# Kernel tuning notes

Measured on AMD Instinct MI355X. Metric: run time of the kernel, lower is better.

Reference implementation:

```python
import jax, jax.numpy as jnp
import numpy as np

B, D, H, E, TOPK = 8192, 1024, 4096, 8, 2


def setup_inputs() -> dict:
    key = jax.random.key(0)
    ks = jax.random.split(key, 5)
    s_in = 1.0 / np.sqrt(D)
    s_h = 1.0 / np.sqrt(H)
    return {
        "x": jax.random.normal(ks[0], (B, D), jnp.float32),
        "Wg": jax.random.normal(ks[1], (D, E), jnp.float32) * s_in,
        "bg": jnp.zeros((E,), jnp.float32),
        "W1": jax.random.normal(ks[2], (E, D, H), jnp.float32) * s_in,
        "b1": jnp.zeros((E, H), jnp.float32),
        "W2": jax.random.normal(ks[3], (E, H, D), jnp.float32) * s_h,
        "b2": jnp.zeros((E, D), jnp.float32),
    }


def reference(x, Wg, bg, W1, b1, W2, b2):
    # Gating: softmax over experts, top-k, renormalize selected weights
    logits = x @ Wg + bg                              # [B, E]
    weights = jax.nn.softmax(logits, axis=-1)
    topw, topi = jax.lax.top_k(weights, TOPK)         # [B, k]
    topw = topw / jnp.sum(topw, axis=-1, keepdims=True)
    # Dense combine weights: [B, E], zero for unselected experts
    comb = jnp.sum(topw[..., None] * jax.nn.one_hot(topi, E, dtype=x.dtype), axis=1)
    # Expert MLPs computed batched per expert (grouped GEMM form)
    h = jax.nn.gelu(jnp.einsum('bd,edh->ebh', x, W1) + b1[:, None, :], approximate=False)  # [E,B,H]
    y = jnp.einsum('ebh,ehd->ebd', h, W2) + b2[:, None, :]                                 # [E,B,D]
    # Weighted combine: only top-k experts have nonzero weight
    out = jnp.einsum('ebd,be->bd', y, comb)           # [B, D]
    return out
```

## Files before the change

kernel.cpp:

```cpp
#include <hip/hip_runtime.h>
#include <stdint.h>

#define B_TOK 8192
#define DDIM 1024
#define HDIM 4096
#define NEXP 8

typedef __bf16 bf16x8 __attribute__((ext_vector_type(8)));
typedef float f32x4 __attribute__((ext_vector_type(4)));

__device__ __forceinline__ unsigned short f2bf(float f) {
  unsigned int u = __float_as_uint(f);
  u += 0x7fffu + ((u >> 16) & 1u);
  return (unsigned short)(u >> 16);
}
__device__ __forceinline__ float bfhi(unsigned int u) {
  return __uint_as_float(u & 0xffff0000u);
}
__device__ __forceinline__ float bflo(unsigned int u) {
  return __uint_as_float(u << 16);
}

__device__ __forceinline__ void gld16(const void* g, void* l) {
  __builtin_amdgcn_global_load_lds(
      (const __attribute__((address_space(1))) void*)g,
      (__attribute__((address_space(3))) void*)l, 16, 0, 0);
}

__device__ __forceinline__ float gelu_f(float v) {
  float u = v * (0.7978845608f + 0.0356774081f * v * v);
  float ex = __expf(2.f * u);
  float th = 1.f - 2.f * __builtin_amdgcn_rcpf(ex + 1.f);
  return 0.5f * v * (1.f + th);
}

__global__ __launch_bounds__(256) void gating_kernel(
    const float* __restrict__ x, const float* __restrict__ Wg,
    const float* __restrict__ bg, int* __restrict__ t2e,
    float* __restrict__ t2w, int* __restrict__ cnt) {
  __shared__ float sWg[NEXP * DDIM];
  int tid = threadIdx.x;
  for (int i = tid; i < NEXP * DDIM; i += 256) {
    int d = i >> 3, e = i & 7;
    sWg[e * DDIM + d] = Wg[i];
  }
  __syncthreads();
  int lane = tid & 63, wave = tid >> 6;
  for (int t = 0; t < 16; ++t) {
    int b = blockIdx.x * 64 + wave * 16 + t;
    float acc[NEXP];
#pragma unroll
    for (int e = 0; e < NEXP; ++e) acc[e] = 0.f;
    const float* xr = x + (size_t)b * DDIM;
#pragma unroll
    for (int j = 0; j < 4; ++j) {
      int d0 = j * 256 + lane * 4;
      float4 xv = *(const float4*)(xr + d0);
#pragma unroll
      for (int e = 0; e < NEXP; ++e) {
        float4 wv = *(const float4*)(sWg + e * DDIM + d0);
        acc[e] += xv.x * wv.x + xv.y * wv.y + xv.z * wv.z + xv.w * wv.w;
      }
    }
#pragma unroll
    for (int off = 32; off > 0; off >>= 1) {
#pragma unroll
      for (int e = 0; e < NEXP; ++e) acc[e] += __shfl_xor(acc[e], off);
    }
    if (lane == 0) {
      float l0[NEXP];
#pragma unroll
      for (int e = 0; e < NEXP; ++e) l0[e] = acc[e] + bg[e];
      int i1 = 0;
      float v1 = l0[0];
#pragma unroll
      for (int e = 1; e < NEXP; ++e)
        if (l0[e] > v1) { v1 = l0[e]; i1 = e; }
      int i2 = (i1 == 0) ? 1 : 0;
      float v2 = l0[i2];
#pragma unroll
      for (int e = 0; e < NEXP; ++e)
        if (e != i1 && l0[e] > v2) { v2 = l0[e]; i2 = e; }
      float w1 = 1.f / (1.f + expf(v2 - v1));
      float w2 = 1.f - w1;
      t2e[b * 2] = i1;
      t2e[b * 2 + 1] = i2;
      t2w[b * 2] = w1;
      t2w[b * 2 + 1] = w2;
      atomicAdd(&cnt[i1], 1);
      atomicAdd(&cnt[i2], 1);
    }
  }
}

__global__ void prefix_kernel(const int* __restrict__ cnt, int* __restrict__ offs,
                              int* __restrict__ tileE, int* __restrict__ tileM,
                              int* __restrict__ ntile) {
  int s = 0, t = 0;
  offs[0] = 0;
  for (int e = 0; e < NEXP; ++e) {
    int c = cnt[e];
    for (int m = 0; m < c; m += 128) { tileE[t] = e; tileM[t] = m; ++t; }
    s += c;
    offs[e + 1] = s;
  }
  *ntile = t;
}

__global__ __launch_bounds__(256) void scatter_kernel(
    const int* __restrict__ t2e, const int* __restrict__ offs,
    int* __restrict__ cursor, int* __restrict__ tok, int* __restrict__ rowpos) {
  int b = blockIdx.x * 256 + threadIdx.x;
  if (b >= B_TOK) return;
#pragma unroll
  for (int k = 0; k < 2; ++k) {
    int e = t2e[b * 2 + k];
    int pos = offs[e] + atomicAdd(&cursor[e], 1);
    tok[pos] = b;
    rowpos[b * 2 + k] = pos;
  }
}

__global__ __launch_bounds__(256) void cvt_x_kernel(const float* __restrict__ x,
                                                    unsigned short* __restrict__ xb) {
  size_t i = ((size_t)blockIdx.x * 256 + threadIdx.x) * 4;
  float4 v = *(const float4*)(x + i);
  ushort4 o;
  o.x = f2bf(v.x);
  o.y = f2bf(v.y);
  o.z = f2bf(v.z);
  o.w = f2bf(v.w);
  *(ushort4*)(xb + i) = o;
}

__global__ __launch_bounds__(256) void transpose_cvt_kernel(
    const float* __restrict__ src, unsigned short* __restrict__ dst, int R, int C) {
  __shared__ unsigned short T[64][72];
  size_t eo = (size_t)blockIdx.z * (size_t)R * C;
  int c0 = blockIdx.x * 64, r0 = blockIdx.y * 64;
  int tid = threadIdx.x;
#pragma unroll
  for (int p = 0; p < 4; ++p) {
    int idx = p * 256 + tid;
    int r = idx >> 4, c4 = (idx & 15) * 4;
    float4 v = *(const float4*)(src + eo + (size_t)(r0 + r) * C + c0 + c4);
    T[r][c4] = f2bf(v.x);
    T[r][c4 + 1] = f2bf(v.y);
    T[r][c4 + 2] = f2bf(v.z);
    T[r][c4 + 3] = f2bf(v.w);
  }
  __syncthreads();
#pragma unroll
  for (int p = 0; p < 2; ++p) {
    int idx = p * 256 + tid;
    int c = idx >> 3, s8 = (idx & 7) * 8;
    ushort4 a, b;
    a.x = T[s8][c];     a.y = T[s8 + 1][c]; a.z = T[s8 + 2][c]; a.w = T[s8 + 3][c];
    b.x = T[s8 + 4][c]; b.y = T[s8 + 5][c]; b.z = T[s8 + 6][c]; b.w = T[s8 + 7][c];
    unsigned short* dp = dst + eo + (size_t)(c0 + c) * R + r0 + s8;
    *(ushort4*)dp = a;
    *(ushort4*)(dp + 4) = b;
  }
}

__global__ __launch_bounds__(256) void gemm1_kernel(
    const unsigned short* __restrict__ xb, const unsigned short* __restrict__ w1t,
    const float* __restrict__ b1, const int* __restrict__ offs,
    const int* __restrict__ tileE, const int* __restrict__ tileM,
    const int* __restrict__ ntile, const int* __restrict__ tok,
    unsigned short* __restrict__ hbuf) {
  int ty = blockIdx.y;
  if (ty >= *ntile) return;
  int e = tileE[ty], m0 = tileM[ty];
  int r0 = offs[e], rows = offs[e + 1] - r0;
  int n0 = blockIdx.x * 128;

  __shared__ __attribute__((aligned(16))) unsigned short Ws[128 * 32];
  __shared__ __attribute__((aligned(16))) unsigned short Xs[128 * 32];

  int tid = threadIdx.x, lane = tid & 63, wave = tid >> 6;
  int u0 = wave * 2, u1 = u0 + 1;
  int sr = lane >> 2, sk = (lane & 3) * 8;
  int nr0 = u0 * 16 + sr, nr1 = u1 * 16 + sr;
  const unsigned short* pW0 = w1t + ((size_t)e * HDIM + n0 + nr0) * DDIM + sk;
  const unsigned short* pW1 = w1t + ((size_t)e * HDIM + n0 + nr1) * DDIM + sk;
  int ma0 = min(m0 + nr0, rows - 1), ma1 = min(m0 + nr1, rows - 1);
  const unsigned short* pX0 = xb + (size_t)tok[r0 + ma0] * DDIM + sk;
  const unsigned short* pX1 = xb + (size_t)tok[r0 + ma1] * DDIM + sk;

  f32x4 acc[4][4];
#pragma unroll
  for (int i = 0; i < 4; ++i)
#pragma unroll
    for (int j = 0; j < 4; ++j) acc[i][j] = (f32x4){0.f, 0.f, 0.f, 0.f};

  int wn = wave & 1, wm = wave >> 1;
  int nbase = wn * 64, mbase = wm * 64;
  int fr = lane & 15, quad = lane >> 4;

  for (int kk = 0; kk < DDIM; kk += 32) {
    gld16(pW0 + kk, Ws + u0 * 512);
    gld16(pW1 + kk, Ws + u1 * 512);
    gld16(pX0 + kk, Xs + u0 * 512);
    gld16(pX1 + kk, Xs + u1 * 512);
    __syncthreads();
    bf16x8 a[4], b[4];
#pragma unroll
    for (int i = 0; i < 4; ++i) {
      a[i] = *(const bf16x8*)(Ws + (size_t)(nbase + i * 16 + fr) * 32 + quad * 8);
      b[i] = *(const bf16x8*)(Xs + (size_t)(mbase + i * 16 + fr) * 32 + quad * 8);
    }
#pragma unroll
    for (int i = 0; i < 4; ++i)
#pragma unroll
      for (int j = 0; j < 4; ++j)
        acc[i][j] = __builtin_amdgcn_mfma_f32_16x16x32_bf16(a[i], b[j], acc[i][j], 0, 0, 0);
    __syncthreads();
  }

  const float* b1e = b1 + (size_t)e * HDIM + n0 + nbase;
  float4 bias[4];
#pragma unroll
  for (int i = 0; i < 4; ++i) bias[i] = *(const float4*)(b1e + i * 16 + quad * 4);
#pragma unroll
  for (int j = 0; j < 4; ++j) {
    int grow = m0 + mbase + j * 16 + fr;
    if (grow < rows) {
      unsigned short* hp = hbuf + (size_t)(r0 + grow) * HDIM + n0 + nbase;
#pragma unroll
      for (int i = 0; i < 4; ++i) {
        ushort4 o;
        o.x = f2bf(gelu_f(acc[i][j][0] + bias[i].x));
        o.y = f2bf(gelu_f(acc[i][j][1] + bias[i].y));
        o.z = f2bf(gelu_f(acc[i][j][2] + bias[i].z));
        o.w = f2bf(gelu_f(acc[i][j][3] + bias[i].w));
        *(ushort4*)(hp + i * 16 + quad * 4) = o;
      }
    }
  }
}

__global__ __launch_bounds__(256) void gemm2_kernel(
    const unsigned short* __restrict__ hbuf, const unsigned short* __restrict__ w2t,
    const float* __restrict__ b2, const int* __restrict__ offs,
    const int* __restrict__ tileE, const int* __restrict__ tileM,
    const int* __restrict__ ntile, unsigned short* __restrict__ ybuf) {
  int ty = blockIdx.y;
  if (ty >= *ntile) return;
  int e = tileE[ty], m0 = tileM[ty];
  int r0 = offs[e], rows = offs[e + 1] - r0;
  int n0 = blockIdx.x * 128;

  __shared__ __attribute__((aligned(16))) unsigned short Ws[128 * 32];
  __shared__ __attribute__((aligned(16))) unsigned short Hs[128 * 32];

  int tid = threadIdx.x, lane = tid & 63, wave = tid >> 6;
  int u0 = wave * 2, u1 = u0 + 1;
  int sr = lane >> 2, sk = (lane & 3) * 8;
  int nr0 = u0 * 16 + sr, nr1 = u1 * 16 + sr;
  const unsigned short* pW0 = w2t + ((size_t)e * DDIM + n0 + nr0) * HDIM + sk;
  const unsigned short* pW1 = w2t + ((size_t)e * DDIM + n0 + nr1) * HDIM + sk;
  const unsigned short* pH0 = hbuf + (size_t)(r0 + min(m0 + nr0, rows - 1)) * HDIM + sk;
  const unsigned short* pH1 = hbuf + (size_t)(r0 + min(m0 + nr1, rows - 1)) * HDIM + sk;

  f32x4 acc[4][4];
#pragma unroll
  for (int i = 0; i < 4; ++i)
#pragma unroll
    for (int j = 0; j < 4; ++j) acc[i][j] = (f32x4){0.f, 0.f, 0.f, 0.f};

  int wn = wave & 1, wm = wave >> 1;
  int nbase = wn * 64, mbase = wm * 64;
  int fr = lane & 15, quad = lane >> 4;

  for (int kk = 0; kk < HDIM; kk += 32) {
    gld16(pW0 + kk, Ws + u0 * 512);
    gld16(pW1 + kk, Ws + u1 * 512);
    gld16(pH0 + kk, Hs + u0 * 512);
    gld16(pH1 + kk, Hs + u1 * 512);
    __syncthreads();
    bf16x8 a[4], b[4];
#pragma unroll
    for (int i = 0; i < 4; ++i) {
      a[i] = *(const bf16x8*)(Ws + (size_t)(nbase + i * 16 + fr) * 32 + quad * 8);
      b[i] = *(const bf16x8*)(Hs + (size_t)(mbase + i * 16 + fr) * 32 + quad * 8);
    }
#pragma unroll
    for (int i = 0; i < 4; ++i)
#pragma unroll
      for (int j = 0; j < 4; ++j)
        acc[i][j] = __builtin_amdgcn_mfma_f32_16x16x32_bf16(a[i], b[j], acc[i][j], 0, 0, 0);
    __syncthreads();
  }

  const float* b2e = b2 + (size_t)e * DDIM + n0 + nbase;
  float4 bias[4];
#pragma unroll
  for (int i = 0; i < 4; ++i) bias[i] = *(const float4*)(b2e + i * 16 + quad * 4);
#pragma unroll
  for (int j = 0; j < 4; ++j) {
    int grow = m0 + mbase + j * 16 + fr;
    if (grow < rows) {
      unsigned short* yp = ybuf + (size_t)(r0 + grow) * DDIM + n0 + nbase;
#pragma unroll
      for (int i = 0; i < 4; ++i) {
        ushort4 o;
        o.x = f2bf(acc[i][j][0] + bias[i].x);
        o.y = f2bf(acc[i][j][1] + bias[i].y);
        o.z = f2bf(acc[i][j][2] + bias[i].z);
        o.w = f2bf(acc[i][j][3] + bias[i].w);
        *(ushort4*)(yp + i * 16 + quad * 4) = o;
      }
    }
  }
}

__global__ __launch_bounds__(256) void combine_kernel(
    const unsigned short* __restrict__ ybuf, const int* __restrict__ rowpos,
    const float* __restrict__ t2w, float* __restrict__ out) {
  int idx = blockIdx.x * 256 + threadIdx.x;
  int b = idx >> 7;
  int c8 = (idx & 127) * 8;
  int p0 = rowpos[b * 2], p1 = rowpos[b * 2 + 1];
  float w0 = t2w[b * 2], w1 = t2w[b * 2 + 1];
  uint4 ya = *(const uint4*)(ybuf + (size_t)p0 * DDIM + c8);
  uint4 yb = *(const uint4*)(ybuf + (size_t)p1 * DDIM + c8);
  float4 o0, o1;
  o0.x = w0 * bflo(ya.x) + w1 * bflo(yb.x);
  o0.y = w0 * bfhi(ya.x) + w1 * bfhi(yb.x);
  o0.z = w0 * bflo(ya.y) + w1 * bflo(yb.y);
  o0.w = w0 * bfhi(ya.y) + w1 * bfhi(yb.y);
  o1.x = w0 * bflo(ya.z) + w1 * bflo(yb.z);
  o1.y = w0 * bfhi(ya.z) + w1 * bfhi(yb.z);
  o1.z = w0 * bflo(ya.w) + w1 * bflo(yb.w);
  o1.w = w0 * bfhi(ya.w) + w1 * bfhi(yb.w);
  float* op = out + (size_t)b * DDIM + c8;
  *(float4*)op = o0;
  *(float4*)(op + 4) = o1;
}

extern "C" void kernel_launch(void* const* d_in, const int* in_sizes, int n_in,
                              void* d_out, int out_size, void* d_ws, size_t ws_size,
                              hipStream_t stream) {
  const float* x = (const float*)d_in[0];
  const float* Wg = (const float*)d_in[1];
  const float* bg = (const float*)d_in[2];
  const float* W1 = (const float*)d_in[3];
  const float* b1 = (const float*)d_in[4];
  const float* W2 = (const float*)d_in[5];
  const float* b2 = (const float*)d_in[6];
  float* out = (float*)d_out;

  char* ws = (char*)d_ws;
  int* cnt = (int*)(ws + 0);
  int* cursor = (int*)(ws + 64);
  int* offs = (int*)(ws + 128);
  int* ntile = (int*)(ws + 192);
  int* tileE = (int*)(ws + 256);
  int* tileM = (int*)(ws + 896);
  int* t2e = (int*)(ws + 2048);
  float* t2w = (float*)(ws + 67584);
  int* tok = (int*)(ws + 133120);
  int* rowpos = (int*)(ws + 198656);
  char* big = ws + 264192;
  unsigned short* xb = (unsigned short*)big;
  unsigned short* w1t = (unsigned short*)(big + 16777216);
  unsigned short* ybuf = w1t;
  unsigned short* w2t = (unsigned short*)(big + 16777216 + 67108864);
  unsigned short* hbuf = (unsigned short*)(big + 16777216 + 2 * 67108864);

  (void)in_sizes; (void)n_in; (void)out_size; (void)ws_size;

  hipMemsetAsync(ws, 0, 256, stream);

  cvt_x_kernel<<<(B_TOK * DDIM) / 1024, 256, 0, stream>>>(x, xb);
  transpose_cvt_kernel<<<dim3(HDIM / 64, DDIM / 64, NEXP), 256, 0, stream>>>(W1, w1t, DDIM, HDIM);
  transpose_cvt_kernel<<<dim3(DDIM / 64, HDIM / 64, NEXP), 256, 0, stream>>>(W2, w2t, HDIM, DDIM);
  gating_kernel<<<B_TOK / 64, 256, 0, stream>>>(x, Wg, bg, t2e, t2w, cnt);
  prefix_kernel<<<1, 1, 0, stream>>>(cnt, offs, tileE, tileM, ntile);
  scatter_kernel<<<B_TOK / 256, 256, 0, stream>>>(t2e, offs, cursor, tok, rowpos);
  gemm1_kernel<<<dim3(HDIM / 128, 136), 256, 0, stream>>>(xb, w1t, b1, offs, tileE, tileM, ntile, tok, hbuf);
  gemm2_kernel<<<dim3(DDIM / 128, 136), 256, 0, stream>>>(hbuf, w2t, b2, offs, tileE, tileM, ntile, ybuf);
  combine_kernel<<<(B_TOK * DDIM) / (256 * 8), 256, 0, stream>>>(ybuf, rowpos, t2w, out);
}
```

Measured before the change: 1.048 ms.

## Double-buffer LDS with BK=64 and XOR swizzle in both expert GEMMs

Both grouped GEMM kernels now load 64-wide K slices into two LDS buffers, so the next slice is prefetched via global_load_lds while MFMAs run on the current one. The barrier count per K drops to one per 64 elements. An XOR swizzle on the 16-byte chunks is meant to avoid LDS bank conflicts on the fragment reads, and launch bounds request two blocks per CU. LDS use grows to 64KB per block, which may limit occupancy, and a single barrier per iteration relies on the load into the other buffer being ordered correctly.

```diff
diff --git a/kernel.cpp b/kernel.cpp
--- a/kernel.cpp
+++ b/kernel.cpp
@@ -14,12 +14,8 @@
   u += 0x7fffu + ((u >> 16) & 1u);
   return (unsigned short)(u >> 16);
 }
-__device__ __forceinline__ float bfhi(unsigned int u) {
-  return __uint_as_float(u & 0xffff0000u);
-}
-__device__ __forceinline__ float bflo(unsigned int u) {
-  return __uint_as_float(u << 16);
-}
+__device__ __forceinline__ float bfhi(unsigned int u) { return __uint_as_float(u & 0xffff0000u); }
+__device__ __forceinline__ float bflo(unsigned int u) { return __uint_as_float(u << 16); }
 
 __device__ __forceinline__ void gld16(const void* g, void* l) {
   __builtin_amdgcn_global_load_lds(
@@ -163,7 +159,8 @@
   }
 }
 
-__global__ __launch_bounds__(256) void gemm1_kernel(
+
+__global__ __launch_bounds__(256, 2) void gemm1_kernel(
     const unsigned short* __restrict__ xb, const unsigned short* __restrict__ w1t,
     const float* __restrict__ b1, const int* __restrict__ offs,
     const int* __restrict__ tileE, const int* __restrict__ tileM,
@@ -175,18 +172,24 @@
   int r0 = offs[e], rows = offs[e + 1] - r0;
   int n0 = blockIdx.x * 128;
 
-  __shared__ __attribute__((aligned(16))) unsigned short Ws[128 * 32];
-  __shared__ __attribute__((aligned(16))) unsigned short Xs[128 * 32];
+  __shared__ __attribute__((aligned(16))) unsigned short Xs[2 * 128 * 64];
+  __shared__ __attribute__((aligned(16))) unsigned short Ws[2 * 128 * 64];
 
   int tid = threadIdx.x, lane = tid & 63, wave = tid >> 6;
-  int u0 = wave * 2, u1 = u0 + 1;
-  int sr = lane >> 2, sk = (lane & 3) * 8;
-  int nr0 = u0 * 16 + sr, nr1 = u1 * 16 + sr;
-  const unsigned short* pW0 = w1t + ((size_t)e * HDIM + n0 + nr0) * DDIM + sk;
-  const unsigned short* pW1 = w1t + ((size_t)e * HDIM + n0 + nr1) * DDIM + sk;
-  int ma0 = min(m0 + nr0, rows - 1), ma1 = min(m0 + nr1, rows - 1);
-  const unsigned short* pX0 = xb + (size_t)tok[r0 + ma0] * DDIM + sk;
-  const unsigned short* pX1 = xb + (size_t)tok[r0 + ma1] * DDIM + sk;
+  int r8 = lane >> 3, c8 = lane & 7;
+  int swb = ((c8 ^ r8) * 16);
+
+  const char* pX[4];
+  const char* pW[4];
+#pragma unroll
+  for (int g = 0; g < 4; ++g) {
+    int rl = wave * 32 + g * 8 + r8;
+    int gr = tok[r0 + min(m0 + rl, rows - 1)];
+    pX[g] = (const char*)(xb + (size_t)gr * DDIM) + swb;
+    pW[g] = (const char*)(w1t + ((size_t)e * HDIM + n0 + rl) * DDIM) + swb;
+  }
+  unsigned short* Xd = Xs + wave * 32 * 64;
+  unsigned short* Wd = Ws + wave * 32 * 64;
 
   f32x4 acc[4][4];
 #pragma unroll
@@ -195,38 +198,55 @@
     for (int j = 0; j < 4; ++j) acc[i][j] = (f32x4){0.f, 0.f, 0.f, 0.f};
 
   int wn = wave & 1, wm = wave >> 1;
-  int nbase = wn * 64, mbase = wm * 64;
   int fr = lane & 15, quad = lane >> 4;
-
-  for (int kk = 0; kk < DDIM; kk += 32) {
-    gld16(pW0 + kk, Ws + u0 * 512);
-    gld16(pW1 + kk, Ws + u1 * 512);
-    gld16(pX0 + kk, Xs + u0 * 512);
-    gld16(pX1 + kk, Xs + u1 * 512);
+  int frb = fr * 64;
+  int q0 = ((quad ^ (fr & 7)) * 8);
+  int q1 = (((quad | 4) ^ (fr & 7)) * 8);
+
+#define STAGE1(buf, kb)                                   \
+  {                                                       \
+    _Pragma("unroll") for (int g = 0; g < 4; ++g) {       \
+      gld16(pX[g] + (kb), Xd + (buf)*8192 + g * 512);     \
+      gld16(pW[g] + (kb), Wd + (buf)*8192 + g * 512);     \
+    }                                                     \
+  }
+
+  STAGE1(0, 0);
+  __syncthreads();
+
+  const int NIT = DDIM / 64;
+  for (int kk = 0; kk < NIT; ++kk) {
+    int cur = kk & 1;
+    if (kk + 1 < NIT) STAGE1(cur ^ 1, (kk + 1) * 128);
+    const unsigned short* Xb = Xs + cur * 8192 + wm * 64 * 64;
+    const unsigned short* Wb = Ws + cur * 8192 + wn * 64 * 64;
+#pragma unroll
+    for (int s = 0; s < 2; ++s) {
+      int qq = s ? q1 : q0;
+      bf16x8 a[4], b[4];
+#pragma unroll
+      for (int i = 0; i < 4; ++i) {
+        a[i] = *(const bf16x8*)(Wb + i * 16 * 64 + frb + qq);
+        b[i] = *(const bf16x8*)(Xb + i * 16 * 64 + frb + qq);
+      }
+#pragma unroll
+      for (int i = 0; i < 4; ++i)
+#pragma unroll
+        for (int j = 0; j < 4; ++j)
+          acc[i][j] = __builtin_amdgcn_mfma_f32_16x16x32_bf16(a[i], b[j], acc[i][j], 0, 0, 0);
+    }
     __syncthreads();
-    bf16x8 a[4], b[4];
-#pragma unroll
-    for (int i = 0; i < 4; ++i) {
-      a[i] = *(const bf16x8*)(Ws + (size_t)(nbase + i * 16 + fr) * 32 + quad * 8);
-      b[i] = *(const bf16x8*)(Xs + (size_t)(mbase + i * 16 + fr) * 32 + quad * 8);
-    }
-#pragma unroll
-    for (int i = 0; i < 4; ++i)
-#pragma unroll
-      for (int j = 0; j < 4; ++j)
-        acc[i][j] = __builtin_amdgcn_mfma_f32_16x16x32_bf16(a[i], b[j], acc[i][j], 0, 0, 0);
-    __syncthreads();
-  }
-
-  const float* b1e = b1 + (size_t)e * HDIM + n0 + nbase;
+  }
+
+  const float* b1e = b1 + (size_t)e * HDIM + n0 + wn * 64;
   float4 bias[4];
 #pragma unroll
   for (int i = 0; i < 4; ++i) bias[i] = *(const float4*)(b1e + i * 16 + quad * 4);
 #pragma unroll
   for (int j = 0; j < 4; ++j) {
-    int grow = m0 + mbase + j * 16 + fr;
+    int grow = m0 + wm * 64 + j * 16 + fr;
     if (grow < rows) {
-      unsigned short* hp = hbuf + (size_t)(r0 + grow) * HDIM + n0 + nbase;
+      unsigned short* hp = hbuf + (size_t)(r0 + grow) * HDIM + n0 + wn * 64;
 #pragma unroll
       for (int i = 0; i < 4; ++i) {
         ushort4 o;
@@ -240,7 +260,7 @@
   }
 }
 
-__global__ __launch_bounds__(256) void gemm2_kernel(
+__global__ __launch_bounds__(256, 2) void gemm2_kernel(
     const unsigned short* __restrict__ hbuf, const unsigned short* __restrict__ w2t,
     const float* __restrict__ b2, const int* __restrict__ offs,
     const int* __restrict__ tileE, const int* __restrict__ tileM,
@@ -251,17 +271,23 @@
   int r0 = offs[e], rows = offs[e + 1] - r0;
   int n0 = blockIdx.x * 128;
 
-  __shared__ __attribute__((aligned(16))) unsigned short Ws[128 * 32];
-  __shared__ __attribute__((aligned(16))) unsigned short Hs[128 * 32];
+  __shared__ __attribute__((aligned(16))) unsigned short Hs[2 * 128 * 64];
+  __shared__ __attribute__((aligned(16))) unsigned short Ws[2 * 128 * 64];
 
   int tid = threadIdx.x, lane = tid & 63, wave = tid >> 6;
-  int u0 = wave * 2, u1 = u0 + 1;
-  int sr = lane >> 2, sk = (lane & 3) * 8;
-  int nr0 = u0 * 16 + sr, nr1 = u1 * 16 + sr;
-  const unsigned short* pW0 = w2t + ((size_t)e * DDIM + n0 + nr0) * HDIM + sk;
-  const unsigned short* pW1 = w2t + ((size_t)e * DDIM + n0 + nr1) * HDIM + sk;
-  const unsigned short* pH0 = hbuf + (size_t)(r0 + min(m0 + nr0, rows - 1)) * HDIM + sk;
-  const unsigned short* pH1 = hbuf + (size_t)(r0 + min(m0 + nr1, rows - 1)) * HDIM + sk;
+  int r8 = lane >> 3, c8 = lane & 7;
+  int swb = ((c8 ^ r8) * 16);
+
+  const char* pH[4];
+  const char* pW[4];
+#pragma unroll
+  for (int g = 0; g < 4; ++g) {
+    int rl = wave * 32 + g * 8 + r8;
+    pH[g] = (const char*)(hbuf + (size_t)(r0 + min(m0 + rl, rows - 1)) * HDIM) + swb;
+    pW[g] = (const char*)(w2t + ((size_t)e * DDIM + n0 + rl) * HDIM) + swb;
+  }
+  unsigned short* Hd = Hs + wave * 32 * 64;
+  unsigned short* Wd = Ws + wave * 32 * 64;
 
   f32x4 acc[4][4];
 #pragma unroll
@@ -270,38 +296,55 @@
     for (int j = 0; j < 4; ++j) acc[i][j] = (f32x4){0.f, 0.f, 0.f, 0.f};
 
   int wn = wave & 1, wm = wave >> 1;
-  int nbase = wn * 64, mbase = wm * 64;
   int fr = lane & 15, quad = lane >> 4;
-
-  for (int kk = 0; kk < HDIM; kk += 32) {
-    gld16(pW0 + kk, Ws + u0 * 512);
-    gld16(pW1 + kk, Ws + u1 * 512);
-    gld16(pH0 + kk, Hs + u0 * 512);
-    gld16(pH1 + kk, Hs + u1 * 512);
+  int frb = fr * 64;
+  int q0 = ((quad ^ (fr & 7)) * 8);
+  int q1 = (((quad | 4) ^ (fr & 7)) * 8);
+
+#define STAGE2(buf, kb)                                   \
+  {                                                       \
+    _Pragma("unroll") for (int g = 0; g < 4; ++g) {       \
+      gld16(pH[g] + (kb), Hd + (buf)*8192 + g * 512);     \
+      gld16(pW[g] + (kb), Wd + (buf)*8192 + g * 512);     \
+    }                                                     \
+  }
+
+  STAGE2(0, 0);
+  __syncthreads();
+
+  const int NIT = HDIM / 64;
+  for (int kk = 0; kk < NIT; ++kk) {
+    int cur = kk & 1;
+    if (kk + 1 < NIT) STAGE2(cur ^ 1, (kk + 1) * 128);
+    const unsigned short* Hb = Hs + cur * 8192 + wm * 64 * 64;
+    const unsigned short* Wb = Ws + cur * 8192 + wn * 64 * 64;
+#pragma unroll
+    for (int s = 0; s < 2; ++s) {
+      int qq = s ? q1 : q0;
+      bf16x8 a[4], b[4];
+#pragma unroll
+      for (int i = 0; i < 4; ++i) {
+        a[i] = *(const bf16x8*)(Wb + i * 16 * 64 + frb + qq);
+        b[i] = *(const bf16x8*)(Hb + i * 16 * 64 + frb + qq);
+      }
+#pragma unroll
+      for (int i = 0; i < 4; ++i)
+#pragma unroll
+        for (int j = 0; j < 4; ++j)
+          acc[i][j] = __builtin_amdgcn_mfma_f32_16x16x32_bf16(a[i], b[j], acc[i][j], 0, 0, 0);
+    }
     __syncthreads();
-    bf16x8 a[4], b[4];
-#pragma unroll
-    for (int i = 0; i < 4; ++i) {
-      a[i] = *(const bf16x8*)(Ws + (size_t)(nbase + i * 16 + fr) * 32 + quad * 8);
-      b[i] = *(const bf16x8*)(Hs + (size_t)(mbase + i * 16 + fr) * 32 + quad * 8);
-    }
-#pragma unroll
-    for (int i = 0; i < 4; ++i)
-#pragma unroll
-      for (int j = 0; j < 4; ++j)
-        acc[i][j] = __builtin_amdgcn_mfma_f32_16x16x32_bf16(a[i], b[j], acc[i][j], 0, 0, 0);
-    __syncthreads();
-  }
-
-  const float* b2e = b2 + (size_t)e * DDIM + n0 + nbase;
+  }
+
+  const float* b2e = b2 + (size_t)e * DDIM + n0 + wn * 64;
   float4 bias[4];
 #pragma unroll
   for (int i = 0; i < 4; ++i) bias[i] = *(const float4*)(b2e + i * 16 + quad * 4);
 #pragma unroll
   for (int j = 0; j < 4; ++j) {
-    int grow = m0 + mbase + j * 16 + fr;
+    int grow = m0 + wm * 64 + j * 16 + fr;
     if (grow < rows) {
-      unsigned short* yp = ybuf + (size_t)(r0 + grow) * DDIM + n0 + nbase;
+      unsigned short* yp = ybuf + (size_t)(r0 + grow) * DDIM + n0 + wn * 64;
 #pragma unroll
       for (int i = 0; i < 4; ++i) {
         ushort4 o;
```

Measured after the change: 1.094 ms. 4.4% more time.
